# Kernel optimization log

Measured on AMD Instinct MI355X. Metric: run time of the kernel, lower is better.

The kernel has to match this reference:

```python
import jax, jax.numpy as jnp
import numpy as np

B, N, L, D = 4, 2048, 12, 128  # batch, nodes, in_len, d_model


def _glorot(key, shape):
    fan_in = shape[0]
    return jax.random.normal(key, shape, dtype=jnp.float32) / jnp.sqrt(jnp.float32(fan_in))


def setup_inputs() -> dict:
    key = jax.random.key(0)
    ks = jax.random.split(key, 12)
    x = jax.random.normal(ks[0], (B, N, L, D), dtype=jnp.float32)
    adj = jax.random.uniform(ks[1], (N, N), dtype=jnp.float32)  # dense weighted adjacency
    # mlp2: Linear(L*D -> D)
    W_mlp2 = _glorot(ks[2], (L * D, D)); b_mlp2 = jnp.zeros((D,), jnp.float32)
    # GNN: three DenseSAGEConv layers (lin_rel on aggregated, lin_root on self)
    Wr1 = _glorot(ks[3], (D, D)); Wo1 = _glorot(ks[4], (D, D)); b1 = jnp.zeros((D,), jnp.float32)
    Wr2 = _glorot(ks[5], (D, D)); Wo2 = _glorot(ks[6], (D, D)); b2 = jnp.zeros((D,), jnp.float32)
    Wr3 = _glorot(ks[7], (D, D)); Wo3 = _glorot(ks[8], (D, D)); b3 = jnp.zeros((D,), jnp.float32)
    # mlp1: Linear(D -> L*D)
    W_mlp1 = _glorot(ks[9], (D, L * D)); b_mlp1 = jnp.zeros((L * D,), jnp.float32)
    return {"x": x, "adj": adj, "W_mlp2": W_mlp2, "b_mlp2": b_mlp2,
            "Wr1": Wr1, "Wo1": Wo1, "b1": b1,
            "Wr2": Wr2, "Wo2": Wo2, "b2": b2,
            "Wr3": Wr3, "Wo3": Wo3, "b3": b3,
            "W_mlp1": W_mlp1, "b_mlp1": b_mlp1}


def reference(x, adj, W_mlp2, b_mlp2, Wr1, Wo1, b1, Wr2, Wo2, b2, Wr3, Wo3, b3, W_mlp1, b_mlp1):
    b_, n_, l_, d_ = x.shape
    xf = x.reshape(b_, n_, l_ * d_)                      # 'b n l d -> b n (l d)'
    h = xf @ W_mlp2 + b_mlp2                             # mlp2: (B,N,D)
    deg = jnp.clip(adj.sum(axis=-1, keepdims=True), 1.0, None)  # (N,1)

    def sage(hin, Wr, Wo, bb):
        # mean neighbor aggregation: (adj @ h) / deg, then rel + root linear
        agg = jnp.einsum('mn,bnd->bmd', adj, hin) / deg
        return agg @ Wr + hin @ Wo + bb

    h = jax.nn.relu(sage(h, Wr1, Wo1, b1))
    h = jax.nn.relu(sage(h, Wr2, Wo2, b2))
    h = sage(h, Wr3, Wo3, b3)                            # gnn1_embed output (B,N,D)
    out = h @ W_mlp1 + b_mlp1                            # mlp1: (B,N,L*D)
    return out
```

## Files before the change

kernel.cpp:

```cpp
#include <hip/hip_runtime.h>

typedef __attribute__((ext_vector_type(8))) short short8;
typedef __attribute__((ext_vector_type(4))) short short4v;
typedef __attribute__((ext_vector_type(4))) float floatx4;

__device__ inline short to_bf16s(float f) {
    unsigned u = __builtin_bit_cast(unsigned, f);
    unsigned r = u + 0x7FFFu + ((u >> 16) & 1u);
    return (short)(r >> 16);
}

__device__ inline void dma16(const short* g, short* l) {
    __builtin_amdgcn_global_load_lds(
        (const __attribute__((address_space(1))) unsigned int*)(const void*)g,
        (__attribute__((address_space(3))) unsigned int*)(void*)l,
        16, 0, 0);
}

template <typename T> struct Ld8;
template <> struct Ld8<short> {
    static __device__ inline short8 load(const short* p) { return *(const short8*)p; }
};
template <> struct Ld8<float> {
    static __device__ inline short8 load(const float* p) {
        float4 f0 = *(const float4*)p;
        float4 f1 = *(const float4*)(p + 4);
        short8 r;
        r[0] = to_bf16s(f0.x); r[1] = to_bf16s(f0.y);
        r[2] = to_bf16s(f0.z); r[3] = to_bf16s(f0.w);
        r[4] = to_bf16s(f1.x); r[5] = to_bf16s(f1.y);
        r[6] = to_bf16s(f1.z); r[7] = to_bf16s(f1.w);
        return r;
    }
};

struct PrepArgs {
    const float* adj;
    const float* W2; const float* W1;
    const float* Wr0; const float* Wo0;
    const float* Wr1; const float* Wo1;
    const float* Wr2; const float* Wo2;
    short* adjS; short* W2T; short* W1T;
    short* BigB0; short* BigB1; short* BigB2;
};

__global__ __launch_bounds__(256) void prepW(PrepArgs p) {
    int t = blockIdx.x;
    __shared__ short tile[32][33];
    int tx = threadIdx.x & 31, ty0 = threadIdx.x >> 5;
    const float* in; int C_; int bx, by;
    short* outp; int outld, copies, copystride, outofs;
    if (t < 192) {
        bx = (t & 3) * 32; by = (t >> 2) * 32; in = p.W2; C_ = 128;
        outp = p.W2T; outld = 1536; copies = 1; copystride = 0; outofs = 0;
    } else if (t < 384) {
        int u = t - 192; bx = (u % 48) * 32; by = (u / 48) * 32; in = p.W1; C_ = 1536;
        outp = p.W1T; outld = 128; copies = 1; copystride = 0; outofs = 0;
    } else {
        int u = t - 384; int l = u / 32; int v = u % 32;
        const float* Wr[3] = {p.Wr0, p.Wr1, p.Wr2};
        const float* Wo[3] = {p.Wo0, p.Wo1, p.Wo2};
        short* BB[3] = {p.BigB0, p.BigB1, p.BigB2};
        outp = BB[l]; outld = 640; C_ = 128;
        if (v < 16) { in = Wr[l]; bx = (v & 3) * 32; by = (v >> 2) * 32;
                      copies = 4; copystride = 128; outofs = 0; }
        else { v -= 16; in = Wo[l]; bx = (v & 3) * 32; by = (v >> 2) * 32;
               copies = 1; copystride = 0; outofs = 512; }
    }
    for (int i = ty0; i < 32; i += 8)
        tile[i][tx] = to_bf16s(in[(size_t)(by + i) * C_ + bx + tx]);
    __syncthreads();
    for (int i = ty0; i < 32; i += 8) {
        short v = tile[tx][i];
        for (int c = 0; c < copies; ++c)
            outp[(size_t)(bx + i) * outld + (by + tx) + outofs + c * copystride] = v;
    }
}

#define LDSTR 72

template <typename TA, int RELU, int ROWMAP, int HTW>
__device__ __forceinline__ void dev_gemmT(
    short* lds, int bidx, int bidy,
    const TA* __restrict__ A, int lda,
    const short* __restrict__ B, int ldb, int kTiles,
    const float* __restrict__ bias,
    short* __restrict__ C, int ldc, int colofs,
    short* __restrict__ HT) {
    int tid = threadIdx.x;
    int blockM = bidx * 32;
    int blockN = bidy * 64;

    int srow = tid >> 3;
    int scol = (tid & 7) * 8;

    const TA* Abase = A + (size_t)blockM * lda;
    const short* Bbase = B + (size_t)blockN * ldb;

    short8 a0_  = Ld8<TA>::load(Abase + (size_t)srow * lda + scol);
    short8 b00_ = Ld8<short>::load(Bbase + (size_t)srow * ldb + scol);
    short8 b10_ = Ld8<short>::load(Bbase + (size_t)(srow + 32) * ldb + scol);
    short8 a1_  = Ld8<TA>::load(Abase + (size_t)srow * lda + 64 + scol);
    short8 b01_ = Ld8<short>::load(Bbase + (size_t)srow * ldb + 64 + scol);
    short8 b11_ = Ld8<short>::load(Bbase + (size_t)(srow + 32) * ldb + 64 + scol);

    floatx4 acc[2];
    #pragma unroll
    for (int j = 0; j < 2; ++j)
        #pragma unroll
        for (int r = 0; r < 4; ++r) acc[j][r] = 0.f;

    int lane = tid & 63;
    int w = tid >> 6;
    int wr = w >> 1, wc = w & 1;
    int quad = lane >> 4, l15 = lane & 15;

    short* buf0 = lds;
    short* buf1 = lds + 96 * LDSTR;

    for (int it = 0; it < kTiles; it += 2) {
        *(short8*)(buf0 + srow * LDSTR + scol) = a0_;
        *(short8*)(buf0 + (32 + srow) * LDSTR + scol) = b00_;
        *(short8*)(buf0 + (64 + srow) * LDSTR + scol) = b10_;
        asm volatile("s_waitcnt lgkmcnt(0)" ::: "memory");
        __builtin_amdgcn_s_barrier();
        if (it + 2 < kTiles) {
            int ko = (it + 2) * 64;
            a0_  = Ld8<TA>::load(Abase + (size_t)srow * lda + ko + scol);
            b00_ = Ld8<short>::load(Bbase + (size_t)srow * ldb + ko + scol);
            b10_ = Ld8<short>::load(Bbase + (size_t)(srow + 32) * ldb + ko + scol);
        }
        {
            const short* Arow = buf0 + (wr * 16 + l15) * LDSTR;
            const short* Brow = buf0 + (32 + wc * 32 + l15) * LDSTR;
            #pragma unroll
            for (int ks = 0; ks < 2; ++ks) {
                int kof = ks * 32 + quad * 8;
                short8 a0 = *(const short8*)(Arow + kof);
                short8 b0 = *(const short8*)(Brow + kof);
                short8 b1 = *(const short8*)(Brow + 16 * LDSTR + kof);
                acc[0] = __builtin_amdgcn_mfma_f32_16x16x32_bf16(a0, b0, acc[0], 0, 0, 0);
                acc[1] = __builtin_amdgcn_mfma_f32_16x16x32_bf16(a0, b1, acc[1], 0, 0, 0);
            }
        }
        *(short8*)(buf1 + srow * LDSTR + scol) = a1_;
        *(short8*)(buf1 + (32 + srow) * LDSTR + scol) = b01_;
        *(short8*)(buf1 + (64 + srow) * LDSTR + scol) = b11_;
        asm volatile("s_waitcnt lgkmcnt(0)" ::: "memory");
        __builtin_amdgcn_s_barrier();
        if (it + 3 < kTiles) {
            int ko = (it + 3) * 64;
            a1_  = Ld8<TA>::load(Abase + (size_t)srow * lda + ko + scol);
            b01_ = Ld8<short>::load(Bbase + (size_t)srow * ldb + ko + scol);
            b11_ = Ld8<short>::load(Bbase + (size_t)(srow + 32) * ldb + ko + scol);
        }
        {
            const short* Arow = buf1 + (wr * 16 + l15) * LDSTR;
            const short* Brow = buf1 + (32 + wc * 32 + l15) * LDSTR;
            #pragma unroll
            for (int ks = 0; ks < 2; ++ks) {
                int kof = ks * 32 + quad * 8;
                short8 a0 = *(const short8*)(Arow + kof);
                short8 b0 = *(const short8*)(Brow + kof);
                short8 b1 = *(const short8*)(Brow + 16 * LDSTR + kof);
                acc[0] = __builtin_amdgcn_mfma_f32_16x16x32_bf16(a0, b0, acc[0], 0, 0, 0);
                acc[1] = __builtin_amdgcn_mfma_f32_16x16x32_bf16(a0, b1, acc[1], 0, 0, 0);
            }
        }
    }

    #pragma unroll
    for (int tj = 0; tj < 2; ++tj) {
        int col = blockN + wc * 32 + tj * 16 + l15;
        float bv = bias[col];
        int m0 = blockM + wr * 16 + quad * 4;
        short4v pk;
        #pragma unroll
        for (int r = 0; r < 4; ++r) {
            int m = m0 + r;
            float xv = acc[tj][r] + bv;
            if (RELU) xv = xv > 0.f ? xv : 0.f;
            short v = to_bf16s(xv);
            pk[r] = v;
            int orow = ROWMAP ? (((m & 2047) << 2) | (m >> 11)) : m;
            C[(size_t)orow * ldc + col + colofs] = v;
            if (HTW && !ROWMAP) {
                HT[(size_t)((m & 3) * 128 + col) * 2048 + (m >> 2)] = v;
            }
        }
        if (HTW && ROWMAP) {
            int b = m0 >> 11, n0 = m0 & 2047;
            *(short4v*)(HT + (size_t)(b * 128 + col) * 2048 + n0) = pk;
        }
    }
}

template <typename TA, int RELU, int ROWMAP, int HTW>
__global__ __launch_bounds__(256) void gemmT(
    const TA* __restrict__ A, int lda,
    const short* __restrict__ B, int ldb, int kTiles,
    const float* __restrict__ bias,
    short* __restrict__ C, int ldc, int colofs,
    short* __restrict__ HT) {
    __shared__ __align__(16) short lds[2 * 96 * LDSTR];
    dev_gemmT<TA, RELU, ROWMAP, HTW>(lds, blockIdx.x, blockIdx.y,
                                     A, lda, B, ldb, kTiles, bias, C, ldc, colofs, HT);
}

__global__ __launch_bounds__(256) void fusedA(PrepArgs p,
                                              const float* __restrict__ x,
                                              const float* __restrict__ b_mlp2,
                                              short* __restrict__ big0,
                                              short* __restrict__ HT) {
    __shared__ __align__(16) short lds[2 * 96 * LDSTR];
    int bid = blockIdx.x;
    if (bid < 512) {
        dev_gemmT<float, 0, 1, 1>(lds, bid & 255, bid >> 8,
                                  x, 1536, p.W2T, 1536, 24, b_mlp2,
                                  big0, 640, 512, HT);
        return;
    }
    int row = bid - 512;
    const float* src = p.adj + (size_t)row * 2048;
    float s = 0.f;
    for (int c = threadIdx.x; c < 2048; c += 256) s += src[c];
    float* red = (float*)lds;
    red[threadIdx.x] = s;
    __syncthreads();
    for (int st = 128; st > 0; st >>= 1) {
        if (threadIdx.x < st) red[threadIdx.x] += red[threadIdx.x + st];
        __syncthreads();
    }
    float d = red[0];
    d = d < 1.f ? 1.f : d;
    float inv = 1.f / d;
    short* dst = p.adjS + (size_t)row * 2048;
    for (int c = threadIdx.x; c < 2048; c += 256) dst[c] = to_bf16s(src[c] * inv);
}

__global__ __launch_bounds__(512) void gemmS(const short* __restrict__ A,
                                             const short* __restrict__ B,
                                             short* __restrict__ C) {
    __shared__ __align__(16) short lds3[3 * 12288];

    int tid = threadIdx.x;
    int kz = blockIdx.z * 512;

    int kswz = (((tid & 7) ^ ((tid >> 3) & 7))) * 8;
    const short* Ab = A + (size_t)(blockIdx.x * 64 + (tid >> 3)) * 2048 + kz + kswz;
    const short* Bb = B + (size_t)(blockIdx.y * 128 + (tid >> 3)) * 2048 + kz + kswz;

    floatx4 acc[4];
    #pragma unroll
    for (int j = 0; j < 4; ++j)
        #pragma unroll
        for (int r = 0; r < 4; ++r) acc[j][r] = 0.f;

    int lane = tid & 63;
    int w = tid >> 6;
    int wr = w & 3, wc = w >> 2;
    int quad = lane >> 4, l15 = lane & 15;

    auto stage = [&](int slot, int it) {
        short* As = lds3 + slot * 12288;
        short* Bs = As + 4096;
        const short* Ag = Ab + it * 64;
        const short* Bg = Bb + it * 64;
        dma16(Ag, As + tid * 8);
        dma16(Bg, Bs + tid * 8);
        dma16(Bg + (size_t)64 * 2048, Bs + tid * 8 + 4096);
    };

    stage(0, 0);
    stage(1, 1);

    int slot = 0;
    for (int it = 0; it < 8; ++it) {
        if (it < 7) asm volatile("s_waitcnt vmcnt(3)" ::: "memory");
        else        asm volatile("s_waitcnt vmcnt(0)" ::: "memory");
        __builtin_amdgcn_s_barrier();
        if (it + 2 < 8) {
            int s2 = slot + 2; if (s2 >= 3) s2 -= 3;
            stage(s2, it + 2);
        }
        const short* As = lds3 + slot * 12288;
        const short* Bs = As + 4096;
        #pragma unroll
        for (int ks = 0; ks < 2; ++ks) {
            int cswz = (((ks * 4 + quad) ^ (l15 & 7))) * 8;
            short8 af = *(const short8*)(As + (wr * 16 + l15) * 64 + cswz);
            short8 bfr[4];
            #pragma unroll
            for (int j = 0; j < 4; ++j)
                bfr[j] = *(const short8*)(Bs + (wc * 64 + j * 16 + l15) * 64 + cswz);
            #pragma unroll
            for (int j = 0; j < 4; ++j)
                acc[j] = __builtin_amdgcn_mfma_f32_16x16x32_bf16(af, bfr[j], acc[j], 0, 0, 0);
        }
        slot = (slot + 1 == 3) ? 0 : slot + 1;
    }

    int colofs = blockIdx.z * 128;
    #pragma unroll
    for (int tj = 0; tj < 4; ++tj) {
        int j = blockIdx.y * 128 + wc * 64 + tj * 16 + l15;
        int jhi = j >> 7, jlo = j & 127;
        int row0 = blockIdx.x * 64 + wr * 16 + quad * 4;
        #pragma unroll
        for (int r = 0; r < 4; ++r) {
            int m = row0 + r;
            C[(size_t)(m * 4 + jhi) * 640 + jlo + colofs] = to_bf16s(acc[tj][r]);
        }
    }
}

__global__ __launch_bounds__(256) void gemmL(
    const short* __restrict__ A, int lda,
    const short* __restrict__ B, int ldb,
    int kChunkIters, const float* __restrict__ bias,
    float* __restrict__ Cf, int ldc) {
    __shared__ __align__(16) short As[128 * 64];
    __shared__ __align__(16) short Bs[128 * 64];

    int tid = threadIdx.x;
    int blockM = blockIdx.x * 128;
    int blockN = blockIdx.y * 128;

    int kswz = (((tid & 7) ^ ((tid >> 3) & 7))) * 8;
    const short* Ab = A + (size_t)(blockM + (tid >> 3)) * lda + kswz;
    const short* Bb = B + (size_t)(blockN + (tid >> 3)) * ldb + kswz;
    short* Al = As + tid * 8;
    short* Bl = Bs + tid * 8;

    floatx4 acc[4][4];
    #pragma unroll
    for (int i = 0; i < 4; ++i)
        #pragma unroll
        for (int j = 0; j < 4; ++j)
            #pragma unroll
            for (int r = 0; r < 4; ++r) acc[i][j][r] = 0.f;

    int lane = tid & 63;
    int w = tid >> 6;
    int wr = w >> 1, wc = w & 1;
    int quad = lane >> 4, l15 = lane & 15;

    for (int it = 0; it < kChunkIters; ++it) {
        const short* Ag = Ab + it * 64;
        const short* Bg = Bb + it * 64;
        #pragma unroll
        for (int r = 0; r < 4; ++r) {
            dma16(Ag + (size_t)r * 32 * lda, Al + r * 2048);
            dma16(Bg + (size_t)r * 32 * ldb, Bl + r * 2048);
        }
        __syncthreads();
        #pragma unroll
        for (int ks = 0; ks < 2; ++ks) {
            int cswz = (((ks * 4 + quad) ^ (l15 & 7))) * 8;
            short8 af[4], bfr[4];
            #pragma unroll
            for (int i = 0; i < 4; ++i)
                af[i] = *(const short8*)(As + (wr * 64 + i * 16 + l15) * 64 + cswz);
            #pragma unroll
            for (int j = 0; j < 4; ++j)
                bfr[j] = *(const short8*)(Bs + (wc * 64 + j * 16 + l15) * 64 + cswz);
            #pragma unroll
            for (int i = 0; i < 4; ++i)
                #pragma unroll
                for (int j = 0; j < 4; ++j)
                    acc[i][j] = __builtin_amdgcn_mfma_f32_16x16x32_bf16(af[i], bfr[j], acc[i][j], 0, 0, 0);
        }
        __syncthreads();
    }

    #pragma unroll
    for (int ti = 0; ti < 4; ++ti) {
        #pragma unroll
        for (int tj = 0; tj < 4; ++tj) {
            int col = blockN + wc * 64 + tj * 16 + l15;
            float bv = bias[col];
            int row0 = blockM + wr * 64 + ti * 16 + quad * 4;
            #pragma unroll
            for (int r = 0; r < 4; ++r) {
                int mp = row0 + r;
                int orow = ((mp & 3) << 11) | (mp >> 2);
                Cf[(size_t)orow * ldc + col] = acc[ti][tj][r] + bv;
            }
        }
    }
}

extern "C" void kernel_launch(void* const* d_in, const int* in_sizes, int n_in,
                              void* d_out, int out_size, void* d_ws, size_t ws_size,
                              hipStream_t stream) {
    const float* x      = (const float*)d_in[0];
    const float* adj    = (const float*)d_in[1];
    const float* W_mlp2 = (const float*)d_in[2];
    const float* b_mlp2 = (const float*)d_in[3];
    const float* Wr1    = (const float*)d_in[4];
    const float* Wo1    = (const float*)d_in[5];
    const float* b1     = (const float*)d_in[6];
    const float* Wr2    = (const float*)d_in[7];
    const float* Wo2    = (const float*)d_in[8];
    const float* b2     = (const float*)d_in[9];
    const float* Wr3    = (const float*)d_in[10];
    const float* Wo3    = (const float*)d_in[11];
    const float* b3     = (const float*)d_in[12];
    const float* W_mlp1 = (const float*)d_in[13];
    const float* b_mlp1 = (const float*)d_in[14];
    float* out = (float*)d_out;

    char* ws = (char*)d_ws;
    size_t off = 0;
    auto alloc = [&](size_t bytes) -> char* {
        char* p = ws + off;
        off = (off + bytes + 255) & ~(size_t)255;
        return p;
    };
    short* W2T  = (short*)alloc(128 * 1536 * 2);
    short* W1T  = (short*)alloc(1536 * 128 * 2);
    short* BigB[3];
    for (int l = 0; l < 3; ++l) BigB[l] = (short*)alloc(128 * 640 * 2);
    short* adjS = (short*)alloc((size_t)2048 * 2048 * 2);
    short* big[4];
    for (int l = 0; l < 4; ++l) big[l] = (short*)alloc((size_t)8192 * 640 * 2);
    short* HT = (short*)alloc((size_t)512 * 2048 * 2);

    dim3 blk(256);

    PrepArgs pa{adj, W_mlp2, W_mlp1, Wr1, Wo1, Wr2, Wo2, Wr3, Wo3,
                adjS, W2T, W1T, BigB[0], BigB[1], BigB[2]};
    prepW<<<480, blk, 0, stream>>>(pa);

    fusedA<<<2560, blk, 0, stream>>>(pa, x, b_mlp2, big[0], HT);

    for (int l = 0; l < 3; ++l) {
        gemmS<<<dim3(32, 4, 4), dim3(512), 0, stream>>>(adjS, HT, big[l]);
        if (l == 0)
            gemmT<short, 1, 0, 1><<<dim3(256, 2), blk, 0, stream>>>(
                big[0], 640, BigB[0], 640, 10, b1, big[1], 640, 512, HT);
        else if (l == 1)
            gemmT<short, 1, 0, 1><<<dim3(256, 2), blk, 0, stream>>>(
                big[1], 640, BigB[1], 640, 10, b2, big[2], 640, 512, HT);
        else
            gemmT<short, 0, 0, 0><<<dim3(256, 2), blk, 0, stream>>>(
                big[2], 640, BigB[2], 640, 10, b3, big[3], 640, 512, nullptr);
    }

    gemmL<<<dim3(64, 12), blk, 0, stream>>>(big[3] + 512, 640, W1T, 128, 2, b_mlp1, out, 1536);
}
```

Before: 211.7 us.

## Use full-width 64x128 tiles for mlp2 GEMM and vectorize adjacency normalization

The mlp2 GEMM previously ran as 512 blocks, each computing a narrower column slice, so the fp32 input x was read more than once. A new dev_gemmM computes all 128 output columns per 64-row block with register-prefetched double buffering, so x (the dominant traffic) is read once. The adjacency row-normalization part now uses float4 loads and packed bf16 stores. The trade-offs are fewer blocks (128 GEMM blocks), which lowers parallelism, and a doubled LDS footprint that may reduce occupancy for the adj blocks sharing the kernel.

```diff
diff --git a/kernel.cpp b/kernel.cpp
--- a/kernel.cpp
+++ b/kernel.cpp
@@ -207,23 +207,162 @@
                                      A, lda, B, ldb, kTiles, bias, C, ldc, colofs, HT);
 }
 
+__device__ __forceinline__ void dev_gemmM(
+    short* lds, int bidx,
+    const float* __restrict__ A,
+    const short* __restrict__ B,
+    const float* __restrict__ bias,
+    short* __restrict__ C,
+    short* __restrict__ HT) {
+    int tid = threadIdx.x;
+    int blockM = bidx * 64;
+
+    int srow = tid >> 3;
+    int scol = (tid & 7) * 8;
+
+    const float* Abase = A + (size_t)blockM * 1536;
+    const short* Bbase = B;
+
+    short8 a0r0_ = Ld8<float>::load(Abase + (size_t)srow * 1536 + scol);
+    short8 a0r1_ = Ld8<float>::load(Abase + (size_t)(srow + 32) * 1536 + scol);
+    short8 b0r0_ = Ld8<short>::load(Bbase + (size_t)srow * 1536 + scol);
+    short8 b0r1_ = Ld8<short>::load(Bbase + (size_t)(srow + 32) * 1536 + scol);
+    short8 b0r2_ = Ld8<short>::load(Bbase + (size_t)(srow + 64) * 1536 + scol);
+    short8 b0r3_ = Ld8<short>::load(Bbase + (size_t)(srow + 96) * 1536 + scol);
+    short8 a1r0_ = Ld8<float>::load(Abase + (size_t)srow * 1536 + 64 + scol);
+    short8 a1r1_ = Ld8<float>::load(Abase + (size_t)(srow + 32) * 1536 + 64 + scol);
+    short8 b1r0_ = Ld8<short>::load(Bbase + (size_t)srow * 1536 + 64 + scol);
+    short8 b1r1_ = Ld8<short>::load(Bbase + (size_t)(srow + 32) * 1536 + 64 + scol);
+    short8 b1r2_ = Ld8<short>::load(Bbase + (size_t)(srow + 64) * 1536 + 64 + scol);
+    short8 b1r3_ = Ld8<short>::load(Bbase + (size_t)(srow + 96) * 1536 + 64 + scol);
+
+    floatx4 acc[2][4];
+    #pragma unroll
+    for (int i = 0; i < 2; ++i)
+        #pragma unroll
+        for (int j = 0; j < 4; ++j)
+            #pragma unroll
+            for (int r = 0; r < 4; ++r) acc[i][j][r] = 0.f;
+
+    int lane = tid & 63;
+    int w = tid >> 6;
+    int wr = w >> 1, wc = w & 1;
+    int quad = lane >> 4, l15 = lane & 15;
+
+    short* buf0 = lds;
+    short* buf1 = lds + 192 * LDSTR;
+
+    for (int it = 0; it < 24; it += 2) {
+        *(short8*)(buf0 + srow * LDSTR + scol) = a0r0_;
+        *(short8*)(buf0 + (32 + srow) * LDSTR + scol) = a0r1_;
+        *(short8*)(buf0 + (64 + srow) * LDSTR + scol) = b0r0_;
+        *(short8*)(buf0 + (96 + srow) * LDSTR + scol) = b0r1_;
+        *(short8*)(buf0 + (128 + srow) * LDSTR + scol) = b0r2_;
+        *(short8*)(buf0 + (160 + srow) * LDSTR + scol) = b0r3_;
+        asm volatile("s_waitcnt lgkmcnt(0)" ::: "memory");
+        __builtin_amdgcn_s_barrier();
+        if (it + 2 < 24) {
+            int ko = (it + 2) * 64;
+            a0r0_ = Ld8<float>::load(Abase + (size_t)srow * 1536 + ko + scol);
+            a0r1_ = Ld8<float>::load(Abase + (size_t)(srow + 32) * 1536 + ko + scol);
+            b0r0_ = Ld8<short>::load(Bbase + (size_t)srow * 1536 + ko + scol);
+            b0r1_ = Ld8<short>::load(Bbase + (size_t)(srow + 32) * 1536 + ko + scol);
+            b0r2_ = Ld8<short>::load(Bbase + (size_t)(srow + 64) * 1536 + ko + scol);
+            b0r3_ = Ld8<short>::load(Bbase + (size_t)(srow + 96) * 1536 + ko + scol);
+        }
+        {
+            const short* Ar = buf0 + (wr * 32 + l15) * LDSTR;
+            const short* Br = buf0 + (64 + wc * 64 + l15) * LDSTR;
+            #pragma unroll
+            for (int ks = 0; ks < 2; ++ks) {
+                int kof = ks * 32 + quad * 8;
+                short8 af0 = *(const short8*)(Ar + kof);
+                short8 af1 = *(const short8*)(Ar + 16 * LDSTR + kof);
+                #pragma unroll
+                for (int j = 0; j < 4; ++j) {
+                    short8 bf = *(const short8*)(Br + j * 16 * LDSTR + kof);
+                    acc[0][j] = __builtin_amdgcn_mfma_f32_16x16x32_bf16(af0, bf, acc[0][j], 0, 0, 0);
+                    acc[1][j] = __builtin_amdgcn_mfma_f32_16x16x32_bf16(af1, bf, acc[1][j], 0, 0, 0);
+                }
+            }
+        }
+        *(short8*)(buf1 + srow * LDSTR + scol) = a1r0_;
+        *(short8*)(buf1 + (32 + srow) * LDSTR + scol) = a1r1_;
+        *(short8*)(buf1 + (64 + srow) * LDSTR + scol) = b1r0_;
+        *(short8*)(buf1 + (96 + srow) * LDSTR + scol) = b1r1_;
+        *(short8*)(buf1 + (128 + srow) * LDSTR + scol) = b1r2_;
+        *(short8*)(buf1 + (160 + srow) * LDSTR + scol) = b1r3_;
+        asm volatile("s_waitcnt lgkmcnt(0)" ::: "memory");
+        __builtin_amdgcn_s_barrier();
+        if (it + 3 < 24) {
+            int ko = (it + 3) * 64;
+            a1r0_ = Ld8<float>::load(Abase + (size_t)srow * 1536 + ko + scol);
+            a1r1_ = Ld8<float>::load(Abase + (size_t)(srow + 32) * 1536 + ko + scol);
+            b1r0_ = Ld8<short>::load(Bbase + (size_t)srow * 1536 + ko + scol);
+            b1r1_ = Ld8<short>::load(Bbase + (size_t)(srow + 32) * 1536 + ko + scol);
+            b1r2_ = Ld8<short>::load(Bbase + (size_t)(srow + 64) * 1536 + ko + scol);
+            b1r3_ = Ld8<short>::load(Bbase + (size_t)(srow + 96) * 1536 + ko + scol);
+        }
+        {
+            const short* Ar = buf1 + (wr * 32 + l15) * LDSTR;
+            const short* Br = buf1 + (64 + wc * 64 + l15) * LDSTR;
+            #pragma unroll
+            for (int ks = 0; ks < 2; ++ks) {
+                int kof = ks * 32 + quad * 8;
+                short8 af0 = *(const short8*)(Ar + kof);
+                short8 af1 = *(const short8*)(Ar + 16 * LDSTR + kof);
+                #pragma unroll
+                for (int j = 0; j < 4; ++j) {
+                    short8 bf = *(const short8*)(Br + j * 16 * LDSTR + kof);
+                    acc[0][j] = __builtin_amdgcn_mfma_f32_16x16x32_bf16(af0, bf, acc[0][j], 0, 0, 0);
+                    acc[1][j] = __builtin_amdgcn_mfma_f32_16x16x32_bf16(af1, bf, acc[1][j], 0, 0, 0);
+                }
+            }
+        }
+    }
+
+    #pragma unroll
+    for (int i = 0; i < 2; ++i) {
+        #pragma unroll
+        for (int j = 0; j < 4; ++j) {
+            int col = wc * 64 + j * 16 + l15;
+            float bv = bias[col];
+            int m0 = blockM + wr * 32 + i * 16 + quad * 4;
+            short4v pk;
+            #pragma unroll
+            for (int r = 0; r < 4; ++r) {
+                int m = m0 + r;
+                float xv = acc[i][j][r] + bv;
+                short v = to_bf16s(xv);
+                pk[r] = v;
+                int orow = ((m & 2047) << 2) | (m >> 11);
+                C[(size_t)orow * 640 + col + 512] = v;
+            }
+            int b = m0 >> 11, n0 = m0 & 2047;
+            *(short4v*)(HT + (size_t)(b * 128 + col) * 2048 + n0) = pk;
+        }
+    }
+}
+
 __global__ __launch_bounds__(256) void fusedA(PrepArgs p,
                                               const float* __restrict__ x,
                                               const float* __restrict__ b_mlp2,
                                               short* __restrict__ big0,
                                               short* __restrict__ HT) {
-    __shared__ __align__(16) short lds[2 * 96 * LDSTR];
+    __shared__ __align__(16) short lds[2 * 192 * LDSTR];
     int bid = blockIdx.x;
-    if (bid < 512) {
-        dev_gemmT<float, 0, 1, 1>(lds, bid & 255, bid >> 8,
-                                  x, 1536, p.W2T, 1536, 24, b_mlp2,
-                                  big0, 640, 512, HT);
+    if (bid < 128) {
+        dev_gemmM(lds, bid, x, p.W2T, b_mlp2, big0, HT);
         return;
     }
-    int row = bid - 512;
+    int row = bid - 128;
     const float* src = p.adj + (size_t)row * 2048;
     float s = 0.f;
-    for (int c = threadIdx.x; c < 2048; c += 256) s += src[c];
+    #pragma unroll
+    for (int v = 0; v < 2; ++v) {
+        float4 f = *(const float4*)(src + (threadIdx.x + v * 256) * 4);
+        s += f.x + f.y + f.z + f.w;
+    }
     float* red = (float*)lds;
     red[threadIdx.x] = s;
     __syncthreads();
@@ -235,7 +374,15 @@
     d = d < 1.f ? 1.f : d;
     float inv = 1.f / d;
     short* dst = p.adjS + (size_t)row * 2048;
-    for (int c = threadIdx.x; c < 2048; c += 256) dst[c] = to_bf16s(src[c] * inv);
+    #pragma unroll
+    for (int v = 0; v < 2; ++v) {
+        int c = (threadIdx.x + v * 256) * 4;
+        float4 f = *(const float4*)(src + c);
+        short4v pk;
+        pk[0] = to_bf16s(f.x * inv); pk[1] = to_bf16s(f.y * inv);
+        pk[2] = to_bf16s(f.z * inv); pk[3] = to_bf16s(f.w * inv);
+        *(short4v*)(dst + c) = pk;
+    }
 }
 
 __global__ __launch_bounds__(512) void gemmS(const short* __restrict__ A,
@@ -432,7 +579,7 @@
                 adjS, W2T, W1T, BigB[0], BigB[1], BigB[2]};
     prepW<<<480, blk, 0, stream>>>(pa);
 
-    fusedA<<<2560, blk, 0, stream>>>(pa, x, b_mlp2, big[0], HT);
+    fusedA<<<2176, blk, 0, stream>>>(pa, x, b_mlp2, big[0], HT);
 
     for (int l = 0; l < 3; ++l) {
         gemmS<<<dim3(32, 4, 4), dim3(512), 0, stream>>>(adjS, HT, big[l]);
```

New measurement: 216.1 us. 2.1% more time.
